# Kernel tuning notes

Measured on AMD Instinct MI355X. Metric: run time of the kernel, lower is better.

## Reference

```python
import jax, jax.numpy as jnp
import numpy as np

B, H, D = 4096, 200, 64
HID = 64


def setup_inputs() -> dict:
    key = jax.random.key(0)
    ks = jax.random.split(key, 12)
    s = 1.0 / np.sqrt(HID)
    return {
        "x": jax.random.normal(ks[0], (B, H, D), jnp.float32),
        "pos_query": jax.random.normal(ks[1], (B, D), jnp.float32),
        "lengths": jax.random.randint(ks[2], (B,), 1, H + 1, jnp.int32),
        "W_ih": jax.random.normal(ks[3], (3 * HID, D), jnp.float32) * s,
        "W_hh": jax.random.normal(ks[4], (3 * HID, HID), jnp.float32) * s,
        "b_ih": jax.random.normal(ks[5], (3 * HID,), jnp.float32) * s,
        "b_hh": jax.random.normal(ks[6], (3 * HID,), jnp.float32) * s,
        "aW_ih": jax.random.normal(ks[7], (3 * HID, HID), jnp.float32) * s,
        "aW_hh": jax.random.normal(ks[8], (3 * HID, HID), jnp.float32) * s,
        "ab_ih": jax.random.normal(ks[9], (3 * HID,), jnp.float32) * s,
        "ab_hh": jax.random.normal(ks[10], (3 * HID,), jnp.float32) * s,
    }


def _gates(x_t, h, W_i, W_h, b_i, b_h):
    gi = x_t @ W_i.T + b_i  # (B, 3H), PyTorch gate order [r, z, n]
    gh = h @ W_h.T + b_h
    gir, giz, gin = jnp.split(gi, 3, axis=-1)
    ghr, ghz, ghn = jnp.split(gh, 3, axis=-1)
    r = jax.nn.sigmoid(gir + ghr)
    z = jax.nn.sigmoid(giz + ghz)
    n = jnp.tanh(gin + r * ghn)
    return z, n


def _forward(x, pos_query, lengths, W_ih, W_hh, b_ih, b_hh, aW_ih, aW_hh, ab_ih, ab_hh):
    # mask[t, b] = True for valid (packed) timesteps
    mask = (jnp.arange(H)[:, None] < lengths[None, :])[:, :, None]  # (H, B, 1)
    xt = jnp.swapaxes(x, 0, 1)  # (H, B, D) time-major

    # --- GRU over packed sequence; padded positions output 0 (pad_packed_sequence) ---
    def gru_step(h, inp):
        x_t, m = inp
        z, n = _gates(x_t, h, W_ih, W_hh, b_ih, b_hh)
        h_new = (1.0 - z) * n + z * h
        h = jnp.where(m, h_new, h)
        return h, jnp.where(m, h_new, 0.0)

    h0 = jnp.zeros((x.shape[0], HID), x.dtype)
    _, out = jax.lax.scan(gru_step, h0, (xt, mask))  # out: (H, B, HID)

    # --- attention over full H (padded scores are 0, matching the torch code) ---
    scores = jnp.einsum("bd,hbd->bh", pos_query, out)  # (B, H)
    att = jax.nn.softmax(scores, axis=1)  # (B, H)

    # --- AUGRU: update gate scaled by attention score, masked to valid steps ---
    att_t = att.T[:, :, None]  # (H, B, 1)

    def augru_step(h, inp):
        o_t, a_t, m = inp
        u, n = _gates(o_t, h, aW_ih, aW_hh, ab_ih, ab_hh)
        u = a_t * u
        h_new = (1.0 - u) * h + u * n
        h = jnp.where(m, h_new, h)
        return h, None

    h_last, _ = jax.lax.scan(augru_step, h0, (out, att_t, mask))
    # h frozen past each sequence's length -> h_last == state at t = length-1
    return h_last  # (B, HID)


def reference(x, pos_query, lengths, W_ih, W_hh, b_ih, b_hh, aW_ih, aW_hh, ab_ih, ab_hh):
    return _forward(x, pos_query, lengths, W_ih, W_hh, b_ih, b_hh,
                    aW_ih, aW_hh, ab_ih, ab_hh)
```

## Files before the change

kernel.cpp:

```cpp
#include <hip/hip_runtime.h>


#define Bq   4096
#define Tq   200
#define BT   16

typedef __attribute__((ext_vector_type(8))) short short8;
typedef __attribute__((ext_vector_type(4))) float f32x4;

#define MFMA(a, b, c) __builtin_amdgcn_mfma_f32_16x16x32_bf16((a), (b), (c), 0, 0, 0)

static __device__ __forceinline__ unsigned short f2bf(float f) {
  unsigned int u = __float_as_uint(f);
  u += 0x7fffu + ((u >> 16) & 1u);
  return (unsigned short)(u >> 16);
}
static __device__ __forceinline__ float bf2f(unsigned short h) {
  return __uint_as_float(((unsigned int)h) << 16);
}
static __device__ __forceinline__ float sigm(float x) {
  return __builtin_amdgcn_rcpf(1.0f + __expf(-x));
}
static __device__ __forceinline__ float tanh_(float x) {
  return 2.0f * __builtin_amdgcn_rcpf(1.0f + __expf(-2.0f * x)) - 1.0f;
}

static __device__ __forceinline__ void split8(f32x4 a, f32x4 b, short8 &hi, short8 &lo) {
#pragma unroll
  for (int i = 0; i < 4; ++i) {
    unsigned short h = f2bf(a[i]);
    hi[i] = (short)h;
    lo[i] = (short)f2bf(a[i] - bf2f(h));
  }
#pragma unroll
  for (int i = 0; i < 4; ++i) {
    unsigned short h = f2bf(b[i]);
    hi[i + 4] = (short)h;
    lo[i + 4] = (short)f2bf(b[i] - bf2f(h));
  }
}

static __device__ __forceinline__ void cvt4(f32x4 v, uint2 &H, uint2 &L) {
  unsigned short h0 = f2bf(v[0]), h1 = f2bf(v[1]), h2 = f2bf(v[2]), h3 = f2bf(v[3]);
  unsigned short l0 = f2bf(v[0] - bf2f(h0)), l1 = f2bf(v[1] - bf2f(h1));
  unsigned short l2 = f2bf(v[2] - bf2f(h2)), l3 = f2bf(v[3] - bf2f(h3));
  H.x = (unsigned)h0 | ((unsigned)h1 << 16);
  H.y = (unsigned)h2 | ((unsigned)h3 << 16);
  L.x = (unsigned)l0 | ((unsigned)l1 << 16);
  L.y = (unsigned)l2 | ((unsigned)l3 << 16);
}

__global__ __launch_bounds__(256, 1)
void gru_fwd(const float* __restrict__ x, const float* __restrict__ pq,
             const int* __restrict__ lengths,
             const float* __restrict__ Wih, const float* __restrict__ Whh,
             const float* __restrict__ bih, const float* __restrict__ bhh,
             unsigned short* __restrict__ outbf,
             float* __restrict__ scores)
{
  __shared__ alignas(16) unsigned short hbH[2][16][72], hbL[2][16][72];
  __shared__ alignas(16) unsigned short xbH[2][16][72], xbL[2][16][72];
  __shared__ float slds[2][4][16];

  const int tid  = threadIdx.x;
  const int w    = tid >> 6;
  const int lane = tid & 63;
  const int c    = lane & 15;
  const int g    = lane >> 4;
  const int jh   = w * 16;
  const int b_g  = blockIdx.x * BT + c;

  const int pb   = tid >> 4;
  const int pd   = 4 * (tid & 15);
  const int pb_g = blockIdx.x * BT + pb;

  for (int i = tid; i < 16 * 72; i += 256) {
    hbH[0][0][i] = 0; hbL[0][0][i] = 0;
  }
  {
    f32x4 xf = *(const f32x4*)(x + (size_t)pb_g * Tq * 64 + pd);
    uint2 H, L; cvt4(xf, H, L);
    *(uint2*)&xbH[0][pb][pd] = H;
    *(uint2*)&xbL[0][pb][pd] = L;
  }

  short8 wiH[3][2], wiL[3][2], whH[3][2], whL[3][2];
#pragma unroll
  for (int gt = 0; gt < 3; ++gt)
#pragma unroll
    for (int kc = 0; kc < 2; ++kc) {
      const float* p = Wih + (size_t)(gt * 64 + jh + c) * 64 + kc * 32 + g * 8;
      split8(*(const f32x4*)p, *(const f32x4*)(p + 4), wiH[gt][kc], wiL[gt][kc]);
      const float* q = Whh + (size_t)(gt * 64 + jh + c) * 64 + kc * 32 + g * 8;
      split8(*(const f32x4*)q, *(const f32x4*)(q + 4), whH[gt][kc], whL[gt][kc]);
    }

  f32x4 bR, bZ, bNi, bNh;
  {
    f32x4 bi0 = *(const f32x4*)(bih + 0 * 64 + jh + 4 * g);
    f32x4 bh0 = *(const f32x4*)(bhh + 0 * 64 + jh + 4 * g);
    f32x4 bi1 = *(const f32x4*)(bih + 1 * 64 + jh + 4 * g);
    f32x4 bh1 = *(const f32x4*)(bhh + 1 * 64 + jh + 4 * g);
    bR = bi0 + bh0; bZ = bi1 + bh1;
    bNi = *(const f32x4*)(bih + 2 * 64 + jh + 4 * g);
    bNh = *(const f32x4*)(bhh + 2 * 64 + jh + 4 * g);
  }
  const f32x4 pqv = *(const f32x4*)(pq + (size_t)b_g * 64 + jh + 4 * g);
  const int len = lengths[b_g];

  f32x4 hreg = {0.f, 0.f, 0.f, 0.f};
  __syncthreads();

  for (int t = 0; t < Tq; ++t) {
    const int cur = t & 1, nxt = cur ^ 1;

    f32x4 xf = {0.f, 0.f, 0.f, 0.f};
    if (t + 1 < Tq)
      xf = *(const f32x4*)(x + (size_t)pb_g * Tq * 64 + (size_t)(t + 1) * 64 + pd);

    short8 xH[2], xL[2], hH[2], hL[2];
#pragma unroll
    for (int kc = 0; kc < 2; ++kc) {
      xH[kc] = *(const short8*)&xbH[cur][c][kc * 32 + g * 8];
      xL[kc] = *(const short8*)&xbL[cur][c][kc * 32 + g * 8];
      hH[kc] = *(const short8*)&hbH[cur][c][kc * 32 + g * 8];
      hL[kc] = *(const short8*)&hbL[cur][c][kc * 32 + g * 8];
    }

    if (t > 0 && w == 0 && lane < 16) {
      float s = slds[nxt][0][lane] + slds[nxt][1][lane] +
                slds[nxt][2][lane] + slds[nxt][3][lane];
      scores[(size_t)(blockIdx.x * BT + lane) * Tq + (t - 1)] = s;
    }

    f32x4 aR = bR, aZ = bZ, aNi = bNi, aNh = bNh;
#pragma unroll
    for (int kc = 0; kc < 2; ++kc) {
      aR = MFMA(wiH[0][kc], xH[kc], aR);
      aR = MFMA(wiH[0][kc], xL[kc], aR);
      aR = MFMA(wiL[0][kc], xH[kc], aR);
      aR = MFMA(whH[0][kc], hH[kc], aR);
      aR = MFMA(whH[0][kc], hL[kc], aR);
      aR = MFMA(whL[0][kc], hH[kc], aR);
      aZ = MFMA(wiH[1][kc], xH[kc], aZ);
      aZ = MFMA(wiH[1][kc], xL[kc], aZ);
      aZ = MFMA(wiL[1][kc], xH[kc], aZ);
      aZ = MFMA(whH[1][kc], hH[kc], aZ);
      aZ = MFMA(whH[1][kc], hL[kc], aZ);
      aZ = MFMA(whL[1][kc], hH[kc], aZ);
      aNi = MFMA(wiH[2][kc], xH[kc], aNi);
      aNi = MFMA(wiH[2][kc], xL[kc], aNi);
      aNi = MFMA(wiL[2][kc], xH[kc], aNi);
      aNh = MFMA(whH[2][kc], hH[kc], aNh);
      aNh = MFMA(whH[2][kc], hL[kc], aNh);
      aNh = MFMA(whL[2][kc], hH[kc], aNh);
    }

    const bool valid = t < len;
    f32x4 outv;
#pragma unroll
    for (int r = 0; r < 4; ++r) {
      float rr = sigm(aR[r]);
      float zz = sigm(aZ[r]);
      float nn = tanh_(aNi[r] + rr * aNh[r]);
      float hn = (1.f - zz) * nn + zz * hreg[r];
      hreg[r] = valid ? hn : hreg[r];
      outv[r] = valid ? hn : 0.f;
    }

    float sp = outv[0] * pqv[0] + outv[1] * pqv[1] + outv[2] * pqv[2] + outv[3] * pqv[3];
    sp += __shfl_xor(sp, 16);
    sp += __shfl_xor(sp, 32);
    if (lane < 16) slds[cur][w][lane] = sp;

    {
      uint2 H, L; cvt4(hreg, H, L);
      *(uint2*)&hbH[nxt][c][jh + 4 * g] = H;
      *(uint2*)&hbL[nxt][c][jh + 4 * g] = L;
    }

    {
      uint2 O;
      O.x = (unsigned)f2bf(outv[0]) | ((unsigned)f2bf(outv[1]) << 16);
      O.y = (unsigned)f2bf(outv[2]) | ((unsigned)f2bf(outv[3]) << 16);
      *(uint2*)(outbf + (size_t)t * Bq * 64 + (size_t)b_g * 64 + jh + 4 * g) = O;
    }

    {
      uint2 H, L; cvt4(xf, H, L);
      *(uint2*)&xbH[nxt][pb][pd] = H;
      *(uint2*)&xbL[nxt][pb][pd] = L;
    }

    __syncthreads();
  }

  if (w == 0 && lane < 16) {
    const int pb2 = (Tq - 1) & 1;
    float s = slds[pb2][0][lane] + slds[pb2][1][lane] +
              slds[pb2][2][lane] + slds[pb2][3][lane];
    scores[(size_t)(blockIdx.x * BT + lane) * Tq + (Tq - 1)] = s;
  }
}

__global__ __launch_bounds__(256)
void softmax_att(const float* __restrict__ scores, float* __restrict__ att)
{
  const int w = threadIdx.x >> 6, lane = threadIdx.x & 63;
  const int row = blockIdx.x * 4 + w;
  const float* s = scores + (size_t)row * Tq;
  float v0 = s[lane], v1 = s[lane + 64], v2 = s[lane + 128];
  float v3 = (lane < Tq - 192) ? s[lane + 192] : -1e30f;
  float m = fmaxf(fmaxf(v0, v1), fmaxf(v2, v3));
#pragma unroll
  for (int off = 32; off >= 1; off >>= 1) m = fmaxf(m, __shfl_xor(m, off));
  float e0 = __expf(v0 - m), e1 = __expf(v1 - m), e2 = __expf(v2 - m);
  float e3 = (lane < Tq - 192) ? __expf(v3 - m) : 0.f;
  float sum = e0 + e1 + e2 + e3;
#pragma unroll
  for (int off = 32; off >= 1; off >>= 1) sum += __shfl_xor(sum, off);
  float inv = 1.f / sum;
  float* a = att + (size_t)row * Tq;
  a[lane] = e0 * inv;
  a[lane + 64] = e1 * inv;
  a[lane + 128] = e2 * inv;
  if (lane < Tq - 192) a[lane + 192] = e3 * inv;
}

__global__ __launch_bounds__(256, 1)
void augru_fwd(const unsigned short* __restrict__ outbf, const float* __restrict__ att,
               const int* __restrict__ lengths,
               const float* __restrict__ Wih, const float* __restrict__ Whh,
               const float* __restrict__ bih, const float* __restrict__ bhh,
               float* __restrict__ hout)
{
  __shared__ alignas(16) unsigned short hbH[2][16][72], hbL[2][16][72];
  __shared__ float att_lds[16][204];

  const int tid  = threadIdx.x;
  const int w    = tid >> 6;
  const int lane = tid & 63;
  const int c    = lane & 15;
  const int g    = lane >> 4;
  const int jh   = w * 16;
  const int b_g  = blockIdx.x * BT + c;

  for (int i = tid; i < 16 * 72; i += 256) {
    hbH[0][0][i] = 0; hbL[0][0][i] = 0;
  }
  for (int i = tid; i < BT * Tq; i += 256)
    att_lds[i / Tq][i % Tq] = att[(size_t)blockIdx.x * BT * Tq + i];

  short8 wiH[3][2], wiL[3][2], whH[3][2], whL[3][2];
#pragma unroll
  for (int gt = 0; gt < 3; ++gt)
#pragma unroll
    for (int kc = 0; kc < 2; ++kc) {
      const float* p = Wih + (size_t)(gt * 64 + jh + c) * 64 + kc * 32 + g * 8;
      split8(*(const f32x4*)p, *(const f32x4*)(p + 4), wiH[gt][kc], wiL[gt][kc]);
      const float* q = Whh + (size_t)(gt * 64 + jh + c) * 64 + kc * 32 + g * 8;
      split8(*(const f32x4*)q, *(const f32x4*)(q + 4), whH[gt][kc], whL[gt][kc]);
    }

  f32x4 bR, bZ, bNi, bNh;
  {
    f32x4 bi0 = *(const f32x4*)(bih + 0 * 64 + jh + 4 * g);
    f32x4 bh0 = *(const f32x4*)(bhh + 0 * 64 + jh + 4 * g);
    f32x4 bi1 = *(const f32x4*)(bih + 1 * 64 + jh + 4 * g);
    f32x4 bh1 = *(const f32x4*)(bhh + 1 * 64 + jh + 4 * g);
    bR = bi0 + bh0; bZ = bi1 + bh1;
    bNi = *(const f32x4*)(bih + 2 * 64 + jh + 4 * g);
    bNh = *(const f32x4*)(bhh + 2 * 64 + jh + 4 * g);
  }
  const int len = lengths[b_g];

  short8 xcur[2];
#pragma unroll
  for (int kc = 0; kc < 2; ++kc)
    xcur[kc] = *(const short8*)(outbf + (size_t)b_g * 64 + kc * 32 + g * 8);

  f32x4 hreg = {0.f, 0.f, 0.f, 0.f};
  __syncthreads();

  for (int t = 0; t < Tq; ++t) {
    const int cur = t & 1, nxt = cur ^ 1;

    short8 xnxt[2];
    if (t + 1 < Tq) {
#pragma unroll
      for (int kc = 0; kc < 2; ++kc)
        xnxt[kc] = *(const short8*)(outbf + (size_t)(t + 1) * Bq * 64 +
                                    (size_t)b_g * 64 + kc * 32 + g * 8);
    } else {
      xnxt[0] = xcur[0]; xnxt[1] = xcur[1];
    }

    short8 hH[2], hL[2];
#pragma unroll
    for (int kc = 0; kc < 2; ++kc) {
      hH[kc] = *(const short8*)&hbH[cur][c][kc * 32 + g * 8];
      hL[kc] = *(const short8*)&hbL[cur][c][kc * 32 + g * 8];
    }
    const float a_t = att_lds[c][t];

    f32x4 aR = bR, aZ = bZ, aNi = bNi, aNh = bNh;
#pragma unroll
    for (int kc = 0; kc < 2; ++kc) {
      aR = MFMA(wiH[0][kc], xcur[kc], aR);
      aR = MFMA(wiL[0][kc], xcur[kc], aR);
      aR = MFMA(whH[0][kc], hH[kc], aR);
      aR = MFMA(whH[0][kc], hL[kc], aR);
      aR = MFMA(whL[0][kc], hH[kc], aR);
      aZ = MFMA(wiH[1][kc], xcur[kc], aZ);
      aZ = MFMA(wiL[1][kc], xcur[kc], aZ);
      aZ = MFMA(whH[1][kc], hH[kc], aZ);
      aZ = MFMA(whH[1][kc], hL[kc], aZ);
      aZ = MFMA(whL[1][kc], hH[kc], aZ);
      aNi = MFMA(wiH[2][kc], xcur[kc], aNi);
      aNi = MFMA(wiL[2][kc], xcur[kc], aNi);
      aNh = MFMA(whH[2][kc], hH[kc], aNh);
      aNh = MFMA(whH[2][kc], hL[kc], aNh);
      aNh = MFMA(whL[2][kc], hH[kc], aNh);
    }

    const bool valid = t < len;
#pragma unroll
    for (int r = 0; r < 4; ++r) {
      float rr = sigm(aR[r]);
      float uu = a_t * sigm(aZ[r]);
      float nn = tanh_(aNi[r] + rr * aNh[r]);
      float hn = (1.f - uu) * hreg[r] + uu * nn;
      hreg[r] = valid ? hn : hreg[r];
    }

    {
      uint2 H, L; cvt4(hreg, H, L);
      *(uint2*)&hbH[nxt][c][jh + 4 * g] = H;
      *(uint2*)&hbL[nxt][c][jh + 4 * g] = L;
    }

    xcur[0] = xnxt[0]; xcur[1] = xnxt[1];
    __syncthreads();
  }

  *(f32x4*)(hout + (size_t)b_g * 64 + jh + 4 * g) = hreg;
}

extern "C" void kernel_launch(void* const* d_in, const int* in_sizes, int n_in,
                              void* d_out, int out_size, void* d_ws, size_t ws_size,
                              hipStream_t stream)
{
  const float* x       = (const float*)d_in[0];
  const float* pq      = (const float*)d_in[1];
  const int*   lengths = (const int*)d_in[2];
  const float* Wih     = (const float*)d_in[3];
  const float* Whh     = (const float*)d_in[4];
  const float* bih     = (const float*)d_in[5];
  const float* bhh     = (const float*)d_in[6];
  const float* aWih    = (const float*)d_in[7];
  const float* aWhh    = (const float*)d_in[8];
  const float* abih    = (const float*)d_in[9];
  const float* abhh    = (const float*)d_in[10];
  float* hout = (float*)d_out;

  char* ws = (char*)d_ws;
  unsigned short* outbf = (unsigned short*)ws;
  float* scores = (float*)(ws + (size_t)Tq * Bq * 64 * 2);
  float* att    = scores + (size_t)Bq * Tq;

  gru_fwd<<<Bq / BT, 256, 0, stream>>>(x, pq, lengths, Wih, Whh, bih, bhh, outbf, scores);
  softmax_att<<<Bq / 4, 256, 0, stream>>>(scores, att);
  augru_fwd<<<Bq / BT, 256, 0, stream>>>(outbf, att, lengths, aWih, aWhh, abih, abhh, hout);
}
```

Before: 569.3 us.

## Halve batch tile to 8 per block, use packed bf16 conversions, allow two blocks/CU

```diff
diff --git a/kernel.cpp b/kernel.cpp
--- a/kernel.cpp
+++ b/kernel.cpp
@@ -1,22 +1,31 @@
 #include <hip/hip_runtime.h>
+#include <hip/hip_bf16.h>
 
 
 #define Bq   4096
 #define Tq   200
-#define BT   16
+#define BT   8
 
 typedef __attribute__((ext_vector_type(8))) short short8;
 typedef __attribute__((ext_vector_type(4))) float f32x4;
 
 #define MFMA(a, b, c) __builtin_amdgcn_mfma_f32_16x16x32_bf16((a), (b), (c), 0, 0, 0)
 
-static __device__ __forceinline__ unsigned short f2bf(float f) {
-  unsigned int u = __float_as_uint(f);
-  u += 0x7fffu + ((u >> 16) & 1u);
-  return (unsigned short)(u >> 16);
-}
-static __device__ __forceinline__ float bf2f(unsigned short h) {
-  return __uint_as_float(((unsigned int)h) << 16);
+static __device__ __forceinline__ unsigned pk2(float a, float b) {
+  __hip_bfloat162 t = __float22bfloat162_rn(make_float2(a, b));
+  unsigned r;
+  __builtin_memcpy(&r, &t, sizeof(r));
+  return r;
+}
+static __device__ __forceinline__ void pack4(f32x4 v, uint2 &H, uint2 &L) {
+  H.x = pk2(v[0], v[1]);
+  H.y = pk2(v[2], v[3]);
+  float l0 = v[0] - __uint_as_float(H.x << 16);
+  float l1 = v[1] - __uint_as_float(H.x & 0xffff0000u);
+  float l2 = v[2] - __uint_as_float(H.y << 16);
+  float l3 = v[3] - __uint_as_float(H.y & 0xffff0000u);
+  L.x = pk2(l0, l1);
+  L.y = pk2(l2, l3);
 }
 static __device__ __forceinline__ float sigm(float x) {
   return __builtin_amdgcn_rcpf(1.0f + __expf(-x));
@@ -24,33 +33,21 @@
 static __device__ __forceinline__ float tanh_(float x) {
   return 2.0f * __builtin_amdgcn_rcpf(1.0f + __expf(-2.0f * x)) - 1.0f;
 }
-
 static __device__ __forceinline__ void split8(f32x4 a, f32x4 b, short8 &hi, short8 &lo) {
-#pragma unroll
-  for (int i = 0; i < 4; ++i) {
-    unsigned short h = f2bf(a[i]);
-    hi[i] = (short)h;
-    lo[i] = (short)f2bf(a[i] - bf2f(h));
-  }
-#pragma unroll
-  for (int i = 0; i < 4; ++i) {
-    unsigned short h = f2bf(b[i]);
-    hi[i + 4] = (short)h;
-    lo[i + 4] = (short)f2bf(b[i] - bf2f(h));
-  }
-}
-
-static __device__ __forceinline__ void cvt4(f32x4 v, uint2 &H, uint2 &L) {
-  unsigned short h0 = f2bf(v[0]), h1 = f2bf(v[1]), h2 = f2bf(v[2]), h3 = f2bf(v[3]);
-  unsigned short l0 = f2bf(v[0] - bf2f(h0)), l1 = f2bf(v[1] - bf2f(h1));
-  unsigned short l2 = f2bf(v[2] - bf2f(h2)), l3 = f2bf(v[3] - bf2f(h3));
-  H.x = (unsigned)h0 | ((unsigned)h1 << 16);
-  H.y = (unsigned)h2 | ((unsigned)h3 << 16);
-  L.x = (unsigned)l0 | ((unsigned)l1 << 16);
-  L.y = (unsigned)l2 | ((unsigned)l3 << 16);
-}
-
-__global__ __launch_bounds__(256, 1)
+  uint2 H, L;
+  pack4(a, H, L);
+  hi[0] = (short)(H.x & 0xffff); hi[1] = (short)(H.x >> 16);
+  hi[2] = (short)(H.y & 0xffff); hi[3] = (short)(H.y >> 16);
+  lo[0] = (short)(L.x & 0xffff); lo[1] = (short)(L.x >> 16);
+  lo[2] = (short)(L.y & 0xffff); lo[3] = (short)(L.y >> 16);
+  pack4(b, H, L);
+  hi[4] = (short)(H.x & 0xffff); hi[5] = (short)(H.x >> 16);
+  hi[6] = (short)(H.y & 0xffff); hi[7] = (short)(H.y >> 16);
+  lo[4] = (short)(L.x & 0xffff); lo[5] = (short)(L.x >> 16);
+  lo[6] = (short)(L.y & 0xffff); lo[7] = (short)(L.y >> 16);
+}
+
+__global__ __launch_bounds__(256, 2)
 void gru_fwd(const float* __restrict__ x, const float* __restrict__ pq,
              const int* __restrict__ lengths,
              const float* __restrict__ Wih, const float* __restrict__ Whh,
@@ -59,8 +56,8 @@
              float* __restrict__ scores)
 {
   __shared__ alignas(16) unsigned short hbH[2][16][72], hbL[2][16][72];
-  __shared__ alignas(16) unsigned short xbH[2][16][72], xbL[2][16][72];
-  __shared__ float slds[2][4][16];
+  __shared__ alignas(16) unsigned short xbH[2][8][72], xbL[2][8][72];
+  __shared__ float slds[2][4][8];
 
   const int tid  = threadIdx.x;
   const int w    = tid >> 6;
@@ -68,20 +65,23 @@
   const int c    = lane & 15;
   const int g    = lane >> 4;
   const int jh   = w * 16;
-  const int b_g  = blockIdx.x * BT + c;
-
-  const int pb   = tid >> 4;
-  const int pd   = 4 * (tid & 15);
+  const int bl   = c & (BT - 1);
+  const int b_g  = blockIdx.x * BT + bl;
+
+  const int pb   = tid >> 5;
+  const int pd   = 2 * (tid & 31);
   const int pb_g = blockIdx.x * BT + pb;
 
   for (int i = tid; i < 16 * 72; i += 256) {
     hbH[0][0][i] = 0; hbL[0][0][i] = 0;
   }
   {
-    f32x4 xf = *(const f32x4*)(x + (size_t)pb_g * Tq * 64 + pd);
-    uint2 H, L; cvt4(xf, H, L);
-    *(uint2*)&xbH[0][pb][pd] = H;
-    *(uint2*)&xbL[0][pb][pd] = L;
+    float2 f = *(const float2*)(x + (size_t)pb_g * Tq * 64 + pd);
+    unsigned H = pk2(f.x, f.y);
+    float l0 = f.x - __uint_as_float(H << 16);
+    float l1 = f.y - __uint_as_float(H & 0xffff0000u);
+    *(unsigned*)&xbH[0][pb][pd] = H;
+    *(unsigned*)&xbL[0][pb][pd] = pk2(l0, l1);
   }
 
   short8 wiH[3][2], wiL[3][2], whH[3][2], whL[3][2];
@@ -114,20 +114,20 @@
   for (int t = 0; t < Tq; ++t) {
     const int cur = t & 1, nxt = cur ^ 1;
 
-    f32x4 xf = {0.f, 0.f, 0.f, 0.f};
+    float2 xf = make_float2(0.f, 0.f);
     if (t + 1 < Tq)
-      xf = *(const f32x4*)(x + (size_t)pb_g * Tq * 64 + (size_t)(t + 1) * 64 + pd);
+      xf = *(const float2*)(x + (size_t)pb_g * Tq * 64 + (size_t)(t + 1) * 64 + pd);
 
     short8 xH[2], xL[2], hH[2], hL[2];
 #pragma unroll
     for (int kc = 0; kc < 2; ++kc) {
-      xH[kc] = *(const short8*)&xbH[cur][c][kc * 32 + g * 8];
-      xL[kc] = *(const short8*)&xbL[cur][c][kc * 32 + g * 8];
+      xH[kc] = *(const short8*)&xbH[cur][bl][kc * 32 + g * 8];
+      xL[kc] = *(const short8*)&xbL[cur][bl][kc * 32 + g * 8];
       hH[kc] = *(const short8*)&hbH[cur][c][kc * 32 + g * 8];
       hL[kc] = *(const short8*)&hbL[cur][c][kc * 32 + g * 8];
     }
 
-    if (t > 0 && w == 0 && lane < 16) {
+    if (t > 0 && w == 0 && lane < BT) {
       float s = slds[nxt][0][lane] + slds[nxt][1][lane] +
                 slds[nxt][2][lane] + slds[nxt][3][lane];
       scores[(size_t)(blockIdx.x * BT + lane) * Tq + (t - 1)] = s;
@@ -168,34 +168,37 @@
       outv[r] = valid ? hn : 0.f;
     }
 
+    {
+      uint2 H, L;
+      pack4(hreg, H, L);
+      *(uint2*)&hbH[nxt][c][jh + 4 * g] = H;
+      *(uint2*)&hbL[nxt][c][jh + 4 * g] = L;
+    }
+
     float sp = outv[0] * pqv[0] + outv[1] * pqv[1] + outv[2] * pqv[2] + outv[3] * pqv[3];
     sp += __shfl_xor(sp, 16);
     sp += __shfl_xor(sp, 32);
-    if (lane < 16) slds[cur][w][lane] = sp;
+    if (lane < BT) slds[cur][w][lane] = sp;
+
+    if (c < BT) {
+      uint2 O;
+      O.x = pk2(outv[0], outv[1]);
+      O.y = pk2(outv[2], outv[3]);
+      *(uint2*)(outbf + (size_t)t * Bq * 64 + (size_t)b_g * 64 + jh + 4 * g) = O;
+    }
 
     {
-      uint2 H, L; cvt4(hreg, H, L);
-      *(uint2*)&hbH[nxt][c][jh + 4 * g] = H;
-      *(uint2*)&hbL[nxt][c][jh + 4 * g] = L;
-    }
-
-    {
-      uint2 O;
-      O.x = (unsigned)f2bf(outv[0]) | ((unsigned)f2bf(outv[1]) << 16);
-      O.y = (unsigned)f2bf(outv[2]) | ((unsigned)f2bf(outv[3]) << 16);
-      *(uint2*)(outbf + (size_t)t * Bq * 64 + (size_t)b_g * 64 + jh + 4 * g) = O;
-    }
-
-    {
-      uint2 H, L; cvt4(xf, H, L);
-      *(uint2*)&xbH[nxt][pb][pd] = H;
-      *(uint2*)&xbL[nxt][pb][pd] = L;
+      unsigned H = pk2(xf.x, xf.y);
+      float l0 = xf.x - __uint_as_float(H << 16);
+      float l1 = xf.y - __uint_as_float(H & 0xffff0000u);
+      *(unsigned*)&xbH[nxt][pb][pd] = H;
+      *(unsigned*)&xbL[nxt][pb][pd] = pk2(l0, l1);
     }
 
     __syncthreads();
   }
 
-  if (w == 0 && lane < 16) {
+  if (w == 0 && lane < BT) {
     const int pb2 = (Tq - 1) & 1;
     float s = slds[pb2][0][lane] + slds[pb2][1][lane] +
               slds[pb2][2][lane] + slds[pb2][3][lane];
@@ -227,7 +230,7 @@
   if (lane < Tq - 192) a[lane + 192] = e3 * inv;
 }
 
-__global__ __launch_bounds__(256, 1)
+__global__ __launch_bounds__(256, 2)
 void augru_fwd(const unsigned short* __restrict__ outbf, const float* __restrict__ att,
                const int* __restrict__ lengths,
                const float* __restrict__ Wih, const float* __restrict__ Whh,
@@ -235,7 +238,7 @@
                float* __restrict__ hout)
 {
   __shared__ alignas(16) unsigned short hbH[2][16][72], hbL[2][16][72];
-  __shared__ float att_lds[16][204];
+  __shared__ float att_lds[BT][204];
 
   const int tid  = threadIdx.x;
   const int w    = tid >> 6;
@@ -243,7 +246,8 @@
   const int c    = lane & 15;
   const int g    = lane >> 4;
   const int jh   = w * 16;
-  const int b_g  = blockIdx.x * BT + c;
+  const int bl   = c & (BT - 1);
+  const int b_g  = blockIdx.x * BT + bl;
 
   for (int i = tid; i < 16 * 72; i += 256) {
     hbH[0][0][i] = 0; hbL[0][0][i] = 0;
@@ -301,7 +305,7 @@
       hH[kc] = *(const short8*)&hbH[cur][c][kc * 32 + g * 8];
       hL[kc] = *(const short8*)&hbL[cur][c][kc * 32 + g * 8];
     }
-    const float a_t = att_lds[c][t];
+    const float a_t = att_lds[bl][t];
 
     f32x4 aR = bR, aZ = bZ, aNi = bNi, aNh = bNh;
 #pragma unroll
@@ -334,7 +338,8 @@
     }
 
     {
-      uint2 H, L; cvt4(hreg, H, L);
+      uint2 H, L;
+      pack4(hreg, H, L);
       *(uint2*)&hbH[nxt][c][jh + 4 * g] = H;
       *(uint2*)&hbL[nxt][c][jh + 4 * g] = L;
     }
@@ -343,7 +348,8 @@
     __syncthreads();
   }
 
-  *(f32x4*)(hout + (size_t)b_g * 64 + jh + 4 * g) = hreg;
+  if (c < BT)
+    *(f32x4*)(hout + (size_t)b_g * 64 + jh + 4 * g) = hreg;
 }
 
 extern "C" void kernel_launch(void* const* d_in, const int* in_sizes, int n_in,
```

Measured after the change: 695.8 us. +22.2%, slower.
